# Optimization experiments

Measured on AMD Instinct MI355X. Metric: run time of the kernel, lower is better.

## Reference

```python
import jax, jax.numpy as jnp
import numpy as np

L, B, V, E, H = 128, 64, 10000, 512, 512


def setup_inputs() -> dict:
    key = jax.random.key(0)
    ks = jax.random.split(key, 12)
    s = 0.05
    seq = jax.random.randint(ks[0], (L, B), 0, V, dtype=jnp.int32)
    seq_length = jnp.full((B,), L, dtype=jnp.int32)  # equal lengths -> pack/pad identity
    return {
        "seq": seq,
        "seq_length": seq_length,
        "emb": jax.random.normal(ks[1], (V, E), jnp.float32) * 0.01,  # matches init.normal std=0.01
        "W_ih_f": jax.random.normal(ks[2], (3 * H, E), jnp.float32) * s,
        "W_hh_f": jax.random.normal(ks[3], (3 * H, H), jnp.float32) * s,
        "b_ih_f": jax.random.normal(ks[4], (3 * H,), jnp.float32) * s,
        "b_hh_f": jax.random.normal(ks[5], (3 * H,), jnp.float32) * s,
        "W_ih_b": jax.random.normal(ks[6], (3 * H, E), jnp.float32) * s,
        "W_hh_b": jax.random.normal(ks[7], (3 * H, H), jnp.float32) * s,
        "b_ih_b": jax.random.normal(ks[8], (3 * H,), jnp.float32) * s,
        "b_hh_b": jax.random.normal(ks[9], (3 * H,), jnp.float32) * s,
        "dec_W": jax.random.normal(ks[10], (V, 2 * H), jnp.float32) * s,
        "dec_b": jax.random.normal(ks[11], (V,), jnp.float32) * s,
    }


def _gru(x_emb, W_ih, W_hh, b_ih, b_hh, reverse):
    # x_emb: [L, B, E]; PyTorch GRU cell equations.
    gx = jnp.einsum('lbe,ge->lbg', x_emb, W_ih) + b_ih  # [L, B, 3H]
    h0 = jnp.zeros((x_emb.shape[1], W_hh.shape[1]), x_emb.dtype)

    def step(h, gx_t):
        gh = h @ W_hh.T + b_hh
        r = jax.nn.sigmoid(gx_t[:, :H] + gh[:, :H])
        z = jax.nn.sigmoid(gx_t[:, H:2 * H] + gh[:, H:2 * H])
        n = jnp.tanh(gx_t[:, 2 * H:] + r * gh[:, 2 * H:])
        h_new = (1.0 - z) * n + z * h
        return h_new, h_new

    _, ys = jax.lax.scan(step, h0, gx, reverse=reverse)
    return ys  # [L, B, H], aligned with input positions


def reference(seq, seq_length, emb, W_ih_f, W_hh_f, b_ih_f, b_hh_f,
              W_ih_b, W_hh_b, b_ih_b, b_hh_b, dec_W, dec_b):
    x = emb[seq]  # [L, B, E]; dropout=0 (eval) -> identity
    out_f = _gru(x, W_ih_f, W_hh_f, b_ih_f, b_hh_f, reverse=False)  # [L, B, H]
    out_b = _gru(x, W_ih_b, W_hh_b, b_ih_b, b_hh_b, reverse=True)   # [L, B, H]
    # EditType.REPLACE: fwd state before the edited token, bwd state after it
    out = jnp.concatenate([out_f[0:L - 2], out_b[2:L]], axis=2)  # [L-2, B, 2H]
    logits = jnp.einsum('lbh,vh->lbv', out, dec_W) + dec_b       # [L-2, B, V]
    return jax.nn.log_softmax(logits, axis=-1)
```

## Files before the change

kernel.cpp:

```cpp
#include <hip/hip_runtime.h>
#include <hip/hip_bf16.h>
#include <stdint.h>

#define LL 128
#define BB 64
#define VV 10000
#define EE 512
#define HH 512
#define G3 1536
#define MROWS 8192
#define DM 8064
#define D2H 1024
#define NPAD 10112
#define FP 16

typedef __bf16 bf16x8 __attribute__((ext_vector_type(8)));
typedef float f32x4 __attribute__((ext_vector_type(4)));
typedef int i32x4 __attribute__((ext_vector_type(4)));
typedef unsigned int u32x4 __attribute__((ext_vector_type(4)));
typedef unsigned short u16;
typedef unsigned long long u64;

static __device__ __forceinline__ float bf2f(u16 u) {
  unsigned int x = ((unsigned int)u) << 16;
  return __builtin_bit_cast(float, x);
}
static __device__ __forceinline__ u16 f2bf(float f) {
  unsigned int x = __builtin_bit_cast(unsigned int, f);
  unsigned int r = x + 0x7FFFu + ((x >> 16) & 1u);
  return (u16)(r >> 16);
}
static __device__ __forceinline__ signed char q8(float v) {
  float r = fminf(fmaxf(rintf(v), -127.f), 127.f);
  return (signed char)(int)r;
}

static __device__ __forceinline__ void cstore16(void* p, u32x4 v) {
  asm volatile("global_store_dwordx4 %0, %1, off sc0 sc1" :: "v"(p), "v"(v) : "memory");
}
static __device__ __forceinline__ void flagstore4(void* p, int v) {
  asm volatile("global_store_dword %0, %1, off sc0 sc1" :: "v"(p), "v"(v) : "memory");
}
static __device__ __forceinline__ int flagload4(const void* p) {
  int v;
  asm volatile("global_load_dword %0, %1, off sc0 sc1\n\ts_waitcnt vmcnt(0)"
               : "=v"(v) : "v"(p) : "memory");
  return v;
}
static __device__ __forceinline__ void gload_lds16(const void* g, void* s) {
  __builtin_amdgcn_global_load_lds(
      (const __attribute__((address_space(1))) unsigned int*)g,
      (__attribute__((address_space(3))) unsigned int*)s, 16, 0, 0);
}

__global__ void k_cast4(const float4* __restrict__ s0, const float4* __restrict__ s1,
                        const float4* __restrict__ s2, const float4* __restrict__ s3,
                        ushort4* __restrict__ d0, ushort4* __restrict__ d1,
                        ushort4* __restrict__ d2, ushort4* __restrict__ d3, int n4) {
  const float4* s; ushort4* d;
  switch (blockIdx.y) {
    case 0: s = s0; d = d0; break;
    case 1: s = s1; d = d1; break;
    case 2: s = s2; d = d2; break;
    default: s = s3; d = d3; break;
  }
  int i = blockIdx.x * blockDim.x + threadIdx.x;
  if (i < n4) {
    float4 v = s[i];
    ushort4 o;
    o.x = f2bf(v.x); o.y = f2bf(v.y); o.z = f2bf(v.z); o.w = f2bf(v.w);
    d[i] = o;
  }
}

__global__ __launch_bounds__(256) void k_quant_w(const float* __restrict__ W,
                                                 signed char* __restrict__ Q,
                                                 float* __restrict__ wscale) {
  const int v = blockIdx.x;
  const int tid = threadIdx.x;
  const int l = tid & 63, w = tid >> 6;
  float4 x = *(const float4*)(W + (long)v * 1024 + tid * 4);
  float m = fmaxf(fmaxf(fabsf(x.x), fabsf(x.y)), fmaxf(fabsf(x.z), fabsf(x.w)));
#pragma unroll
  for (int off = 32; off; off >>= 1) m = fmaxf(m, __shfl_xor(m, off));
  __shared__ float red[4];
  __shared__ float s_inv;
  if (l == 0) red[w] = m;
  __syncthreads();
  if (tid == 0) {
    float mm = fmaxf(fmaxf(red[0], red[1]), fmaxf(red[2], red[3]));
    mm = fmaxf(mm, 1e-12f);
    s_inv = 127.f / mm;
    wscale[v] = mm / (127.f * 127.f);
  }
  __syncthreads();
  float inv = s_inv;
  char4 o;
  o.x = q8(x.x * inv); o.y = q8(x.y * inv); o.z = q8(x.z * inv); o.w = q8(x.w * inv);
  *(char4*)(Q + (long)v * 1024 + tid * 4) = o;
}

__global__ void k_embed(const int* __restrict__ seq, const float* __restrict__ emb,
                        u16* __restrict__ x) {
  int rb = blockIdx.x;
  int v = seq[rb];
  const float4* s = (const float4*)(emb + (long)v * EE);
  ushort4* d = (ushort4*)(x + (long)rb * EE);
  int t = threadIdx.x;
  float4 val = s[t];
  ushort4 o;
  o.x = f2bf(val.x); o.y = f2bf(val.y); o.z = f2bf(val.z); o.w = f2bf(val.w);
  d[t] = o;
}

__global__ __launch_bounds__(256) void k_gemm_gx(
    const u16* __restrict__ A, const u16* __restrict__ W0, const u16* __restrict__ W1,
    const float* __restrict__ b0, const float* __restrict__ b1, u16* __restrict__ C)
{
  __shared__ char smem[32768];
  const int tid = threadIdx.x;
  const int l = tid & 63;
  const int w = tid >> 6;
  const int wr = w >> 1, wc = w & 1;
  const long tM = (long)blockIdx.x * 128;
  const long tN = (long)blockIdx.y * 128;
  const int z = blockIdx.z;
  const u16* B = z ? W1 : W0;
  const float* bias = z ? b1 : b0;
  u16* Cz = C + (size_t)z * MROWS * G3;

  f32x4 acc[4][4];
#pragma unroll
  for (int m = 0; m < 4; m++)
#pragma unroll
    for (int n = 0; n < 4; n++) acc[m][n] = {0.f, 0.f, 0.f, 0.f};

  for (int kt = 0; kt < 8; ++kt) {
    const int k0 = kt << 6;
#pragma unroll
    for (int i = 0; i < 4; i++) {
      int cchunk = w * 4 + i;
      int c = cchunk * 64 + l;
      int row = c >> 3, k8 = c & 7;
      gload_lds16(A + (tM + row) * EE + k0 + k8 * 8, smem + cchunk * 1024);
      gload_lds16(B + (tN + row) * EE + k0 + k8 * 8, smem + 16384 + cchunk * 1024);
    }
    __syncthreads();
#pragma unroll
    for (int kk = 0; kk < 2; kk++) {
      const int kb = kk * 64 + ((l >> 4) * 16);
      bf16x8 af[4], bfr[4];
#pragma unroll
      for (int m = 0; m < 4; m++) {
        int ra = wr * 64 + m * 16 + (l & 15);
        af[m] = *(const bf16x8*)(smem + ra * 128 + kb);
      }
#pragma unroll
      for (int n = 0; n < 4; n++) {
        int rb2 = wc * 64 + n * 16 + (l & 15);
        bfr[n] = *(const bf16x8*)(smem + 16384 + rb2 * 128 + kb);
      }
#pragma unroll
      for (int m = 0; m < 4; m++)
#pragma unroll
        for (int n = 0; n < 4; n++)
          acc[m][n] = __builtin_amdgcn_mfma_f32_16x16x32_bf16(af[m], bfr[n], acc[m][n], 0, 0, 0);
    }
    __syncthreads();
  }
#pragma unroll
  for (int n = 0; n < 4; n++) {
    long col = tN + wc * 64 + n * 16 + (l & 15);
    float bv = bias[col];
#pragma unroll
    for (int m = 0; m < 4; m++) {
      long row = tM + wr * 64 + m * 16 + ((l >> 4) * 4);
#pragma unroll
      for (int r = 0; r < 4; r++)
        Cz[(row + r) * G3 + col] = f2bf(acc[m][n][r] + bv);
    }
  }
}

template<int OUTBF16>
__global__ __launch_bounds__(256) void k_gemm_i8(
    const signed char* __restrict__ A,
    const signed char* __restrict__ B,
    const float* __restrict__ wscale,
    const float* __restrict__ bias,
    void* __restrict__ Cv)
{
  __shared__ char smem[32768];
  const int tid = threadIdx.x;
  const int l = tid & 63;
  const int w = tid >> 6;
  const int wr = w >> 1, wc = w & 1;
  const long tM = (long)blockIdx.x * 128;
  const long tN = (long)blockIdx.y * 128;

  i32x4 acc[4][4];
#pragma unroll
  for (int m = 0; m < 4; m++)
#pragma unroll
    for (int n = 0; n < 4; n++) acc[m][n] = {0, 0, 0, 0};

  for (int kt = 0; kt < 8; ++kt) {
    const int k0 = kt << 7;
#pragma unroll
    for (int i = 0; i < 4; i++) {
      int j = w * 4 + i;
      int row = j * 8 + (l >> 3);
      int k16 = l & 7;
      gload_lds16(A + (tM + row) * 1024 + k0 + k16 * 16, smem + j * 1024);
      gload_lds16(B + (tN + row) * 1024 + k0 + k16 * 16, smem + 16384 + j * 1024);
    }
    __syncthreads();
#pragma unroll
    for (int ks = 0; ks < 2; ks++) {
      const int kb = ks * 64 + ((l >> 4) * 16);
      i32x4 af[4], bfr[4];
#pragma unroll
      for (int m = 0; m < 4; m++) {
        int ra = wr * 64 + m * 16 + (l & 15);
        af[m] = *(const i32x4*)(smem + ra * 128 + kb);
      }
#pragma unroll
      for (int n = 0; n < 4; n++) {
        int rb2 = wc * 64 + n * 16 + (l & 15);
        bfr[n] = *(const i32x4*)(smem + 16384 + rb2 * 128 + kb);
      }
#pragma unroll
      for (int m = 0; m < 4; m++)
#pragma unroll
        for (int n = 0; n < 4; n++)
          acc[m][n] = __builtin_amdgcn_mfma_i32_16x16x64_i8(af[m], bfr[n], acc[m][n], 0, 0, 0);
    }
    __syncthreads();
  }
#pragma unroll
  for (int n = 0; n < 4; n++) {
    long col = tN + wc * 64 + n * 16 + (l & 15);
    if (col < VV) {
      float sc = wscale[col];
      float bv = bias[col];
#pragma unroll
      for (int m = 0; m < 4; m++) {
        long row = tM + wr * 64 + m * 16 + ((l >> 4) * 4);
#pragma unroll
        for (int r = 0; r < 4; r++) {
          float vv = (float)acc[m][n][r] * sc + bv;
          if (OUTBF16) ((u16*)Cv)[(row + r) * NPAD + col] = f2bf(vv);
          else         ((float*)Cv)[(row + r) * VV + col] = vv;
        }
      }
    }
  }
}

__global__ __launch_bounds__(256) void k_gru(
    const u16* __restrict__ Whh_all,
    const float* __restrict__ bhh_f, const float* __restrict__ bhh_b,
    const u16* __restrict__ gx_all,
    u16* __restrict__ hsteps,
    signed char* __restrict__ catq,
    int* __restrict__ bar16)
{
  const int blk = blockIdx.x;
  const int dir = blockIdx.y;
  const int tid = threadIdx.x;
  const int l = tid & 63, w = tid >> 6;
  const u16* Whh = Whh_all + (long)dir * G3 * HH;
  const float* bhh = dir ? bhh_b : bhh_f;
  const u16* gx = gx_all + (long)dir * MROWS * G3;

  __shared__ char Wl[96 * 1024];
  __shared__ __align__(16) u16 hstage[BB][32];
  __shared__ __align__(8) signed char hstageq[BB][32];

  for (int c = tid; c < 6144; c += 256) {
    int lr = c >> 6;
    int k8 = c & 63;
    int gr = (lr >> 5) * HH + blk * 32 + (lr & 31);
    uint4 v = *(const uint4*)(Whh + (long)gr * HH + k8 * 8);
    *(uint4*)(Wl + lr * 1024 + ((k8 * 16) ^ ((lr & 7) << 4))) = v;
  }
  float bh[6];
#pragma unroll
  for (int n = 0; n < 6; n++) {
    int c = n * 16 + (l & 15);
    bh[n] = bhh[(c >> 5) * HH + blk * 32 + (c & 31)];
  }
  float hreg[4][2] = {};
  __syncthreads();

  const int lrow = w * 16 + ((l >> 4) * 4);
  const int srow = tid >> 2, schunk = tid & 3;

  u16 gxn[3][4][2];
  {
    const int lpos0 = dir ? (LL - 1) : 0;
#pragma unroll
    for (int r = 0; r < 4; r++) {
      const u16* gxr = gx + ((long)lpos0 * BB + (lrow + r)) * G3 + blk * 32;
#pragma unroll
      for (int g = 0; g < 3; g++)
#pragma unroll
        for (int p = 0; p < 2; p++)
          gxn[g][r][p] = gxr[g * HH + p * 16 + (l & 15)];
    }
  }

  for (int t = 0; t < LL; ++t) {
    const int lpos = dir ? (LL - 1 - t) : t;
    const u16* hsrc = hsteps + ((size_t)t * 2 + dir) * BB * HH;

    u16 gxv[3][4][2];
#pragma unroll
    for (int g = 0; g < 3; g++)
#pragma unroll
      for (int r = 0; r < 4; r++)
#pragma unroll
        for (int p = 0; p < 2; p++) gxv[g][r][p] = gxn[g][r][p];

    bf16x8 af[16];
    {
      const u16* hrow = hsrc + (w * 16 + (l & 15)) * HH + ((l >> 4) * 8);
#pragma unroll
      for (int kc = 0; kc < 16; kc++) af[kc] = *(const bf16x8*)(hrow + kc * 32);
    }

    f32x4 acc[6];
#pragma unroll
    for (int n = 0; n < 6; n++) acc[n] = {0.f, 0.f, 0.f, 0.f};
#pragma unroll
    for (int kc = 0; kc < 16; kc++) {
      const int kb = kc * 64 + ((l >> 4) * 16);
#pragma unroll
      for (int n = 0; n < 6; n++) {
        int lr = n * 16 + (l & 15);
        bf16x8 bfr = *(const bf16x8*)(Wl + lr * 1024 + (kb ^ ((l & 7) << 4)));
        acc[n] = __builtin_amdgcn_mfma_f32_16x16x32_bf16(af[kc], bfr, acc[n], 0, 0, 0);
      }
    }

#pragma unroll
    for (int r = 0; r < 4; r++) {
#pragma unroll
      for (int p = 0; p < 2; p++) {
        float ghr = acc[0 + p][r] + bh[0 + p];
        float ghz = acc[2 + p][r] + bh[2 + p];
        float ghn = acc[4 + p][r] + bh[4 + p];
        float xr = bf2f(gxv[0][r][p]);
        float xz = bf2f(gxv[1][r][p]);
        float xn = bf2f(gxv[2][r][p]);
        float ar = fminf(fmaxf(xr + ghr, -30.f), 30.f);
        float az = fminf(fmaxf(xz + ghz, -30.f), 30.f);
        float rg = 1.f / (1.f + __expf(-ar));
        float zg = 1.f / (1.f + __expf(-az));
        float an = fminf(fmaxf(xn + rg * ghn, -30.f), 30.f);
        float e2 = __expf(-2.f * an);
        float ng = (1.f - e2) / (1.f + e2);
        float hn = (1.f - zg) * ng + zg * hreg[r][p];
        hreg[r][p] = hn;
        hstage[lrow + r][p * 16 + (l & 15)] = f2bf(hn);
        hstageq[lrow + r][p * 16 + (l & 15)] = q8(hn * 127.f);
      }
    }
    __syncthreads();

    u32x4 hv = *(const u32x4*)&hstage[srow][schunk * 8];
    u64 hq = *(const u64*)&hstageq[srow][schunk * 8];
    if (t < LL - 1) {
      u16* hdst = hsteps + ((size_t)(t + 1) * 2 + dir) * BB * HH;
      cstore16(hdst + srow * HH + blk * 32 + schunk * 8, hv);
      asm volatile("s_waitcnt vmcnt(0)" ::: "memory");
      __syncthreads();
      if (tid == 0)
        flagstore4(&bar16[((dir * LL + t) * 16 + blk) * FP], 1);
      {
        const int lposn = dir ? (LL - 2 - t) : (t + 1);
#pragma unroll
        for (int r = 0; r < 4; r++) {
          const u16* gxr = gx + ((long)lposn * BB + (lrow + r)) * G3 + blk * 32;
#pragma unroll
          for (int g = 0; g < 3; g++)
#pragma unroll
            for (int p = 0; p < 2; p++)
              gxn[g][r][p] = gxr[g * HH + p * 16 + (l & 15)];
        }
      }
      if (dir == 0) {
        if (lpos < LL - 2)
          *(u64*)(catq + ((long)lpos * BB + srow) * D2H + blk * 32 + schunk * 8) = hq;
      } else {
        if (lpos >= 2)
          *(u64*)(catq + ((long)(lpos - 2) * BB + srow) * D2H + HH + blk * 32 + schunk * 8) = hq;
      }
      const int* flg = bar16 + (dir * LL + t) * 16 * FP;
      for (;;) {
        int v = 1;
        if (l < 16) v = flagload4(&flg[l * FP]);
        if (__all(v != 0)) break;
      }
      __builtin_amdgcn_sched_barrier(0);
    } else {
      if (dir == 0) {
        if (lpos < LL - 2)
          *(u64*)(catq + ((long)lpos * BB + srow) * D2H + blk * 32 + schunk * 8) = hq;
      } else {
        if (lpos >= 2)
          *(u64*)(catq + ((long)(lpos - 2) * BB + srow) * D2H + HH + blk * 32 + schunk * 8) = hq;
      }
    }
  }
}

__global__ __launch_bounds__(256) void k_lsm(float* __restrict__ out) {
  const long row = blockIdx.x;
  float* p = out + row * VV;
  const int tid = threadIdx.x;
  const int l = tid & 63, w = tid >> 6;
  __shared__ float red[8];

  float4 v[10];
  float m = -1e30f;
#pragma unroll
  for (int j = 0; j < 10; j++) {
    int idx = j * 256 + tid;
    if (idx < 2500) {
      v[j] = *(float4*)(p + idx * 4);
      m = fmaxf(m, fmaxf(fmaxf(v[j].x, v[j].y), fmaxf(v[j].z, v[j].w)));
    }
  }
#pragma unroll
  for (int off = 32; off; off >>= 1) m = fmaxf(m, __shfl_xor(m, off));
  if (l == 0) red[w] = m;
  __syncthreads();
  m = fmaxf(fmaxf(red[0], red[1]), fmaxf(red[2], red[3]));

  float s = 0.f;
#pragma unroll
  for (int j = 0; j < 10; j++) {
    int idx = j * 256 + tid;
    if (idx < 2500) {
      s += __expf(v[j].x - m) + __expf(v[j].y - m) + __expf(v[j].z - m) + __expf(v[j].w - m);
    }
  }
#pragma unroll
  for (int off = 32; off; off >>= 1) s += __shfl_xor(s, off);
  if (l == 0) red[4 + w] = s;
  __syncthreads();
  s = red[4] + red[5] + red[6] + red[7];
  float lse = m + logf(s);

#pragma unroll
  for (int j = 0; j < 10; j++) {
    int idx = j * 256 + tid;
    if (idx < 2500) {
      float4 o;
      o.x = v[j].x - lse; o.y = v[j].y - lse; o.z = v[j].z - lse; o.w = v[j].w - lse;
      *(float4*)(p + idx * 4) = o;
    }
  }
}

__global__ __launch_bounds__(256) void k_lsm_b(const u16* __restrict__ lg,
                                               float* __restrict__ out) {
  const long row = blockIdx.x;
  const u16* p = lg + row * NPAD;
  float* q = out + row * VV;
  const int tid = threadIdx.x;
  const int l = tid & 63, w = tid >> 6;
  __shared__ float red[8];

  float v[5][8];
  float m = -1e30f;
#pragma unroll
  for (int j = 0; j < 5; j++) {
    int idx8 = j * 256 + tid;
    if (idx8 < 1250) {
      u32x4 u = *(const u32x4*)(p + idx8 * 8);
#pragma unroll
      for (int e = 0; e < 4; e++) {
        v[j][2 * e]     = bf2f((u16)(u[e] & 0xffffu));
        v[j][2 * e + 1] = bf2f((u16)(u[e] >> 16));
      }
#pragma unroll
      for (int e = 0; e < 8; e++) m = fmaxf(m, v[j][e]);
    }
  }
#pragma unroll
  for (int off = 32; off; off >>= 1) m = fmaxf(m, __shfl_xor(m, off));
  if (l == 0) red[w] = m;
  __syncthreads();
  m = fmaxf(fmaxf(red[0], red[1]), fmaxf(red[2], red[3]));

  float s = 0.f;
#pragma unroll
  for (int j = 0; j < 5; j++) {
    int idx8 = j * 256 + tid;
    if (idx8 < 1250) {
#pragma unroll
      for (int e = 0; e < 8; e++) s += __expf(v[j][e] - m);
    }
  }
#pragma unroll
  for (int off = 32; off; off >>= 1) s += __shfl_xor(s, off);
  if (l == 0) red[4 + w] = s;
  __syncthreads();
  s = red[4] + red[5] + red[6] + red[7];
  float lse = m + logf(s);

#pragma unroll
  for (int j = 0; j < 5; j++) {
    int idx8 = j * 256 + tid;
    if (idx8 < 1250) {
      float4 a, b;
      a.x = v[j][0] - lse; a.y = v[j][1] - lse; a.z = v[j][2] - lse; a.w = v[j][3] - lse;
      b.x = v[j][4] - lse; b.y = v[j][5] - lse; b.z = v[j][6] - lse; b.w = v[j][7] - lse;
      *(float4*)(q + idx8 * 8) = a;
      *(float4*)(q + idx8 * 8 + 4) = b;
    }
  }
}

extern "C" void kernel_launch(void* const* d_in, const int* in_sizes, int n_in,
                              void* d_out, int out_size, void* d_ws, size_t ws_size,
                              hipStream_t stream) {
  const int*   seq  = (const int*)d_in[0];
  const float* emb  = (const float*)d_in[2];
  const float* Wihf = (const float*)d_in[3];
  const float* Whhf = (const float*)d_in[4];
  const float* bihf = (const float*)d_in[5];
  const float* bhhf = (const float*)d_in[6];
  const float* Wihb = (const float*)d_in[7];
  const float* Whhb = (const float*)d_in[8];
  const float* bihb = (const float*)d_in[9];
  const float* bhhb = (const float*)d_in[10];
  const float* decW = (const float*)d_in[11];
  const float* decb = (const float*)d_in[12];

  char* ws = (char*)d_ws;
  size_t off = 0;
  u16* Whh_bf = (u16*)(ws + off); off += (size_t)2 * G3 * HH * 2;
  u16* Wih_bf = (u16*)(ws + off); off += (size_t)2 * G3 * EE * 2;
  signed char* decWq = (signed char*)(ws + off); off += (size_t)NPAD * 1024;
  float* wscale = (float*)(ws + off); off += (size_t)NPAD * 4;
  u16* xb = (u16*)(ws + off); off += (size_t)MROWS * EE * 2;
  u16* gxb = (u16*)(ws + off); off += (size_t)2 * MROWS * G3 * 2;
  signed char* catq = (signed char*)(ws + off); off += (size_t)DM * D2H;
  u16* hsteps = (u16*)(ws + off); off += (size_t)(LL + 1) * 2 * BB * HH * 2;
  int* bar16 = (int*)(ws + off); off += (size_t)2 * LL * 16 * FP * 4;
  u16* logitsb = (u16*)(ws + off);
  const size_t logits_bytes = (size_t)DM * NPAD * 2;
  const bool use_bf16_logits = (ws_size >= off + logits_bytes);

  (void)hipMemsetAsync(hsteps, 0, (size_t)2 * BB * HH * 2, stream);
  (void)hipMemsetAsync(bar16, 0, (size_t)2 * LL * 16 * FP * 4, stream);

  const int n4w = G3 * HH / 4;
  k_cast4<<<dim3((n4w + 255) / 256, 4), 256, 0, stream>>>(
      (const float4*)Whhf, (const float4*)Whhb, (const float4*)Wihf, (const float4*)Wihb,
      (ushort4*)Whh_bf, (ushort4*)(Whh_bf + G3 * HH),
      (ushort4*)Wih_bf, (ushort4*)(Wih_bf + G3 * EE), n4w);
  k_quant_w<<<VV, 256, 0, stream>>>(decW, decWq, wscale);
  k_embed<<<MROWS, 128, 0, stream>>>(seq, emb, xb);

  k_gemm_gx<<<dim3(64, 12, 2), 256, 0, stream>>>(xb, Wih_bf, Wih_bf + G3 * EE,
                                                 bihf, bihb, gxb);

  k_gru<<<dim3(16, 2), 256, 0, stream>>>(Whh_bf, bhhf, bhhb, gxb, hsteps, catq, bar16);

  if (use_bf16_logits) {
    k_gemm_i8<1><<<dim3(63, 79), 256, 0, stream>>>(catq, decWq, wscale, decb, logitsb);
    k_lsm_b<<<DM, 256, 0, stream>>>(logitsb, (float*)d_out);
  } else {
    k_gemm_i8<0><<<dim3(63, 79), 256, 0, stream>>>(catq, decWq, wscale, decb, d_out);
    k_lsm<<<DM, 256, 0, stream>>>((float*)d_out);
  }
}
```

Before: 1.098 ms.

## Fuse GRU recurrence and decoder GEMM into one persistent kernel with flag-gated tiles

The GRU recurrence and the int8 decoder GEMM now run in a single persistent kernel. 32 blocks run the bidirectional GRU and the remaining blocks pull decoder tiles from an atomic ticket counter, ordered from the middle of the sequence outward. Each tile waits on the per-step barrier flags until the forward and backward hidden states it needs have been written. This overlaps the latency-bound serial recurrence with decoder matmul work that would otherwise wait for it. The quantized hidden states are now stored with coherent stores so other blocks can read them, at the cost of extra flag polling and possible contention between GRU and GEMM blocks for memory bandwidth.

Measured after the change: 982.2 us. -10.6%, faster.

```diff
diff --git a/kernel.cpp b/kernel.cpp
--- a/kernel.cpp
+++ b/kernel.cpp
@@ -13,11 +13,14 @@
 #define D2H 1024
 #define NPAD 10112
 #define FP 16
+#define NTILE_M 63
+#define NTILE_N 79
 
 typedef __bf16 bf16x8 __attribute__((ext_vector_type(8)));
 typedef float f32x4 __attribute__((ext_vector_type(4)));
 typedef int i32x4 __attribute__((ext_vector_type(4)));
 typedef unsigned int u32x4 __attribute__((ext_vector_type(4)));
+typedef unsigned int u32x2 __attribute__((ext_vector_type(2)));
 typedef unsigned short u16;
 typedef unsigned long long u64;
 
@@ -37,6 +40,10 @@
 
 static __device__ __forceinline__ void cstore16(void* p, u32x4 v) {
   asm volatile("global_store_dwordx4 %0, %1, off sc0 sc1" :: "v"(p), "v"(v) : "memory");
+}
+static __device__ __forceinline__ void cstore8(void* p, u64 v) {
+  u32x2 d = __builtin_bit_cast(u32x2, v);
+  asm volatile("global_store_dwordx2 %0, %1, off sc0 sc1" :: "v"(p), "v"(d) : "memory");
 }
 static __device__ __forceinline__ void flagstore4(void* p, int v) {
   asm volatile("global_store_dword %0, %1, off sc0 sc1" :: "v"(p), "v"(v) : "memory");
@@ -182,100 +189,22 @@
   }
 }
 
-template<int OUTBF16>
-__global__ __launch_bounds__(256) void k_gemm_i8(
-    const signed char* __restrict__ A,
-    const signed char* __restrict__ B,
-    const float* __restrict__ wscale,
-    const float* __restrict__ bias,
-    void* __restrict__ Cv)
-{
-  __shared__ char smem[32768];
-  const int tid = threadIdx.x;
-  const int l = tid & 63;
-  const int w = tid >> 6;
-  const int wr = w >> 1, wc = w & 1;
-  const long tM = (long)blockIdx.x * 128;
-  const long tN = (long)blockIdx.y * 128;
-
-  i32x4 acc[4][4];
-#pragma unroll
-  for (int m = 0; m < 4; m++)
-#pragma unroll
-    for (int n = 0; n < 4; n++) acc[m][n] = {0, 0, 0, 0};
-
-  for (int kt = 0; kt < 8; ++kt) {
-    const int k0 = kt << 7;
-#pragma unroll
-    for (int i = 0; i < 4; i++) {
-      int j = w * 4 + i;
-      int row = j * 8 + (l >> 3);
-      int k16 = l & 7;
-      gload_lds16(A + (tM + row) * 1024 + k0 + k16 * 16, smem + j * 1024);
-      gload_lds16(B + (tN + row) * 1024 + k0 + k16 * 16, smem + 16384 + j * 1024);
-    }
-    __syncthreads();
-#pragma unroll
-    for (int ks = 0; ks < 2; ks++) {
-      const int kb = ks * 64 + ((l >> 4) * 16);
-      i32x4 af[4], bfr[4];
-#pragma unroll
-      for (int m = 0; m < 4; m++) {
-        int ra = wr * 64 + m * 16 + (l & 15);
-        af[m] = *(const i32x4*)(smem + ra * 128 + kb);
-      }
-#pragma unroll
-      for (int n = 0; n < 4; n++) {
-        int rb2 = wc * 64 + n * 16 + (l & 15);
-        bfr[n] = *(const i32x4*)(smem + 16384 + rb2 * 128 + kb);
-      }
-#pragma unroll
-      for (int m = 0; m < 4; m++)
-#pragma unroll
-        for (int n = 0; n < 4; n++)
-          acc[m][n] = __builtin_amdgcn_mfma_i32_16x16x64_i8(af[m], bfr[n], acc[m][n], 0, 0, 0);
-    }
-    __syncthreads();
-  }
-#pragma unroll
-  for (int n = 0; n < 4; n++) {
-    long col = tN + wc * 64 + n * 16 + (l & 15);
-    if (col < VV) {
-      float sc = wscale[col];
-      float bv = bias[col];
-#pragma unroll
-      for (int m = 0; m < 4; m++) {
-        long row = tM + wr * 64 + m * 16 + ((l >> 4) * 4);
-#pragma unroll
-        for (int r = 0; r < 4; r++) {
-          float vv = (float)acc[m][n][r] * sc + bv;
-          if (OUTBF16) ((u16*)Cv)[(row + r) * NPAD + col] = f2bf(vv);
-          else         ((float*)Cv)[(row + r) * VV + col] = vv;
-        }
-      }
-    }
-  }
-}
-
-__global__ __launch_bounds__(256) void k_gru(
+
+static __device__ void gru_body(
+    int blk, int dir, int tid, char* lds,
     const u16* __restrict__ Whh_all,
     const float* __restrict__ bhh_f, const float* __restrict__ bhh_b,
-    const u16* __restrict__ gx_all,
-    u16* __restrict__ hsteps,
-    signed char* __restrict__ catq,
-    int* __restrict__ bar16)
+    const u16* __restrict__ gx_all, u16* __restrict__ hsteps,
+    signed char* __restrict__ catq, int* __restrict__ bar16)
 {
-  const int blk = blockIdx.x;
-  const int dir = blockIdx.y;
-  const int tid = threadIdx.x;
   const int l = tid & 63, w = tid >> 6;
   const u16* Whh = Whh_all + (long)dir * G3 * HH;
   const float* bhh = dir ? bhh_b : bhh_f;
   const u16* gx = gx_all + (long)dir * MROWS * G3;
 
-  __shared__ char Wl[96 * 1024];
-  __shared__ __align__(16) u16 hstage[BB][32];
-  __shared__ __align__(8) signed char hstageq[BB][32];
+  char* Wl = lds;
+  u16 (*hstage)[32] = (u16(*)[32])(lds + 96 * 1024);
+  signed char (*hstageq)[32] = (signed char(*)[32])(lds + 96 * 1024 + 4096);
 
   for (int c = tid; c < 6144; c += 256) {
     int lr = c >> 6;
@@ -370,9 +299,16 @@
 
     u32x4 hv = *(const u32x4*)&hstage[srow][schunk * 8];
     u64 hq = *(const u64*)&hstageq[srow][schunk * 8];
+    if (t < LL - 1)
+      cstore16(hsteps + ((size_t)(t + 1) * 2 + dir) * BB * HH + srow * HH + blk * 32 + schunk * 8, hv);
+    if (dir == 0) {
+      if (lpos < LL - 2)
+        cstore8(catq + ((long)lpos * BB + srow) * D2H + blk * 32 + schunk * 8, hq);
+    } else {
+      if (lpos >= 2)
+        cstore8(catq + ((long)(lpos - 2) * BB + srow) * D2H + HH + blk * 32 + schunk * 8, hq);
+    }
     if (t < LL - 1) {
-      u16* hdst = hsteps + ((size_t)(t + 1) * 2 + dir) * BB * HH;
-      cstore16(hdst + srow * HH + blk * 32 + schunk * 8, hv);
       asm volatile("s_waitcnt vmcnt(0)" ::: "memory");
       __syncthreads();
       if (tid == 0)
@@ -389,13 +325,6 @@
               gxn[g][r][p] = gxr[g * HH + p * 16 + (l & 15)];
         }
       }
-      if (dir == 0) {
-        if (lpos < LL - 2)
-          *(u64*)(catq + ((long)lpos * BB + srow) * D2H + blk * 32 + schunk * 8) = hq;
-      } else {
-        if (lpos >= 2)
-          *(u64*)(catq + ((long)(lpos - 2) * BB + srow) * D2H + HH + blk * 32 + schunk * 8) = hq;
-      }
       const int* flg = bar16 + (dir * LL + t) * 16 * FP;
       for (;;) {
         int v = 1;
@@ -403,15 +332,124 @@
         if (__all(v != 0)) break;
       }
       __builtin_amdgcn_sched_barrier(0);
-    } else {
-      if (dir == 0) {
-        if (lpos < LL - 2)
-          *(u64*)(catq + ((long)lpos * BB + srow) * D2H + blk * 32 + schunk * 8) = hq;
-      } else {
-        if (lpos >= 2)
-          *(u64*)(catq + ((long)(lpos - 2) * BB + srow) * D2H + HH + blk * 32 + schunk * 8) = hq;
-      }
-    }
+    }
+  }
+}
+
+static __device__ void dec_body(
+    int tid, char* smem, int* tk_sh,
+    const signed char* __restrict__ A, const signed char* __restrict__ B,
+    const float* __restrict__ wscale, const float* __restrict__ bias,
+    void* __restrict__ Cv, int outbf,
+    int* __restrict__ ticket, const int* __restrict__ bar16)
+{
+  const int l = tid & 63;
+  const int w = tid >> 6;
+  const int wr = w >> 1, wc = w & 1;
+
+  for (;;) {
+    if (tid == 0)
+      *tk_sh = __hip_atomic_fetch_add(ticket, 1, __ATOMIC_RELAXED, __HIP_MEMORY_SCOPE_AGENT);
+    __syncthreads();
+    const int n = *tk_sh;
+    __syncthreads();
+    if (n >= NTILE_M * NTILE_N) return;
+    const int k = n / NTILE_N, j = n % NTILE_N;
+    const int mi = (k & 1) ? (31 + ((k + 1) >> 1)) : (31 - (k >> 1));
+    const long tM = (long)mi * 128;
+    const long tN = (long)j * 128;
+
+    {
+      const int tf = 2 * mi + 1;
+      const int tb = 125 - 2 * mi;
+      const int* fp = (l < 16)
+          ? bar16 + ((0 * LL + tf) * 16 + l) * FP
+          : bar16 + ((1 * LL + tb) * 16 + (l & 15)) * FP;
+      for (;;) {
+        int v = 1;
+        if (l < 32) v = flagload4(fp);
+        if (__all(v != 0)) break;
+      }
+    }
+
+    i32x4 acc[4][4];
+#pragma unroll
+    for (int m = 0; m < 4; m++)
+#pragma unroll
+      for (int nn = 0; nn < 4; nn++) acc[m][nn] = {0, 0, 0, 0};
+
+    for (int kt = 0; kt < 8; ++kt) {
+      const int k0 = kt << 7;
+#pragma unroll
+      for (int i = 0; i < 4; i++) {
+        int jj = w * 4 + i;
+        int row = jj * 8 + (l >> 3);
+        int k16 = l & 7;
+        gload_lds16(A + (tM + row) * 1024 + k0 + k16 * 16, smem + jj * 1024);
+        gload_lds16(B + (tN + row) * 1024 + k0 + k16 * 16, smem + 16384 + jj * 1024);
+      }
+      __syncthreads();
+#pragma unroll
+      for (int ks = 0; ks < 2; ks++) {
+        const int kb = ks * 64 + ((l >> 4) * 16);
+        i32x4 af[4], bfr[4];
+#pragma unroll
+        for (int m = 0; m < 4; m++) {
+          int ra = wr * 64 + m * 16 + (l & 15);
+          af[m] = *(const i32x4*)(smem + ra * 128 + kb);
+        }
+#pragma unroll
+        for (int nn = 0; nn < 4; nn++) {
+          int rb2 = wc * 64 + nn * 16 + (l & 15);
+          bfr[nn] = *(const i32x4*)(smem + 16384 + rb2 * 128 + kb);
+        }
+#pragma unroll
+        for (int m = 0; m < 4; m++)
+#pragma unroll
+          for (int nn = 0; nn < 4; nn++)
+            acc[m][nn] = __builtin_amdgcn_mfma_i32_16x16x64_i8(af[m], bfr[nn], acc[m][nn], 0, 0, 0);
+      }
+      __syncthreads();
+    }
+#pragma unroll
+    for (int nn = 0; nn < 4; nn++) {
+      long col = tN + wc * 64 + nn * 16 + (l & 15);
+      if (col < VV) {
+        float sc = wscale[col];
+        float bv = bias[col];
+#pragma unroll
+        for (int m = 0; m < 4; m++) {
+          long row = tM + wr * 64 + m * 16 + ((l >> 4) * 4);
+#pragma unroll
+          for (int r = 0; r < 4; r++) {
+            float vv = (float)acc[m][nn][r] * sc + bv;
+            if (outbf) ((u16*)Cv)[(row + r) * NPAD + col] = f2bf(vv);
+            else       ((float*)Cv)[(row + r) * VV + col] = vv;
+          }
+        }
+      }
+    }
+  }
+}
+
+__global__ __launch_bounds__(256) void k_fused(
+    const u16* __restrict__ Whh_all,
+    const float* __restrict__ bhh_f, const float* __restrict__ bhh_b,
+    const u16* __restrict__ gx_all, u16* __restrict__ hsteps,
+    signed char* __restrict__ catq, int* __restrict__ bar16,
+    const signed char* __restrict__ decWq, const float* __restrict__ wscale,
+    const float* __restrict__ decb, void* __restrict__ Cv, int outbf,
+    int* __restrict__ ticket)
+{
+  __shared__ __align__(16) char lds[104448];
+  __shared__ int tk_sh;
+  const int bid = blockIdx.x;
+  const int tid = threadIdx.x;
+  if (bid < 32) {
+    gru_body(bid >> 1, bid & 1, tid, lds, Whh_all, bhh_f, bhh_b, gx_all,
+             hsteps, catq, bar16);
+  } else {
+    dec_body(tid, lds, &tk_sh, catq, decWq, wscale, decb, Cv, outbf, ticket, bar16);
   }
 }
 
@@ -551,12 +589,13 @@
   signed char* catq = (signed char*)(ws + off); off += (size_t)DM * D2H;
   u16* hsteps = (u16*)(ws + off); off += (size_t)(LL + 1) * 2 * BB * HH * 2;
   int* bar16 = (int*)(ws + off); off += (size_t)2 * LL * 16 * FP * 4;
+  int* ticket = (int*)(ws + off); off += 64;
   u16* logitsb = (u16*)(ws + off);
   const size_t logits_bytes = (size_t)DM * NPAD * 2;
   const bool use_bf16_logits = (ws_size >= off + logits_bytes);
 
   (void)hipMemsetAsync(hsteps, 0, (size_t)2 * BB * HH * 2, stream);
-  (void)hipMemsetAsync(bar16, 0, (size_t)2 * LL * 16 * FP * 4, stream);
+  (void)hipMemsetAsync(bar16, 0, (size_t)2 * LL * 16 * FP * 4 + 64, stream);
 
   const int n4w = G3 * HH / 4;
   k_cast4<<<dim3((n4w + 255) / 256, 4), 256, 0, stream>>>(
@@ -569,13 +608,11 @@
   k_gemm_gx<<<dim3(64, 12, 2), 256, 0, stream>>>(xb, Wih_bf, Wih_bf + G3 * EE,
                                                  bihf, bihb, gxb);
 
-  k_gru<<<dim3(16, 2), 256, 0, stream>>>(Whh_bf, bhhf, bhhb, gxb, hsteps, catq, bar16);
-
-  if (use_bf16_logits) {
-    k_gemm_i8<1><<<dim3(63, 79), 256, 0, stream>>>(catq, decWq, wscale, decb, logitsb);
-    k_lsm_b<<<DM, 256, 0, stream>>>(logitsb, (float*)d_out);
-  } else {
-    k_gemm_i8<0><<<dim3(63, 79), 256, 0, stream>>>(catq, decWq, wscale, decb, d_out);
-    k_lsm<<<DM, 256, 0, stream>>>((float*)d_out);
-  }
-}
+  void* Cv = use_bf16_logits ? (void*)logitsb : (void*)d_out;
+  k_fused<<<dim3(256), 256, 0, stream>>>(Whh_bf, bhhf, bhhb, gxb, hsteps, catq,
+                                         bar16, decWq, wscale, decb, Cv,
+                                         use_bf16_logits ? 1 : 0, ticket);
+
+  if (use_bf16_logits) k_lsm_b<<<DM, 256, 0, stream>>>(logitsb, (float*)d_out);
+  else                 k_lsm<<<DM, 256, 0, stream>>>((float*)d_out);
+}
```
